# Kernel tuning notes

Measured on AMD Instinct MI355X. Metric: run time of the kernel, lower is better.

Reference implementation:

```python
import jax, jax.numpy as jnp
import numpy as np

ENC = 768
DEC = 768
B, T, S = 16, 1024, 1024


def setup_inputs() -> dict:
    key = jax.random.key(0)
    k1, k2, k3 = jax.random.split(key, 3)
    inputs = jax.random.normal(k1, (B, T, DEC), dtype=jnp.float32)
    context = jax.random.normal(k2, (B, S, ENC), dtype=jnp.float32)
    # linear_out: Linear(dec+enc -> dec) with bias; torch weight layout [out, in]
    W_out = jax.random.normal(k3, (DEC, DEC + ENC), dtype=jnp.float32) * 0.02
    b_out = jnp.zeros((DEC,), dtype=jnp.float32)
    w_scale = jnp.ones((1, 1, 1), dtype=jnp.float32)   # self.weight
    b_scale = jnp.ones((1, 1, 1), dtype=jnp.float32)   # self.bias
    prelu_a = jnp.full((1,), 0.25, dtype=jnp.float32)  # PReLU single param
    return {"inputs": inputs, "context": context, "W_out": W_out,
            "b_out": b_out, "w_scale": w_scale, "b_scale": b_scale,
            "prelu_a": prelu_a}


def reference(inputs, context, W_out, b_out, w_scale, b_scale, prelu_a):
    # score: bmm(h_t, h_s^T). NOTE: linear_in output is discarded in the
    # original (h_t reassigned), so the raw inputs are used — faithful here.
    align = jnp.einsum('btd,bsd->bts', inputs, context)        # [B,T,S]
    av = jax.nn.softmax(align, axis=-1)                        # softmax over src
    # gate: sigmoid of per-source column-sum over target positions
    gate = jax.nn.sigmoid(jnp.sum(av, axis=1, keepdims=True))  # [B,1,S]
    # AdaptiveAvgPool1d(1): mean over last (src) dim -> [B,T,1]
    pooled = jnp.mean(av, axis=-1, keepdims=True)
    av_g = av * gate * pooled                                  # fused elementwise
    c = jnp.einsum('bts,bsd->btd', av_g, context)              # [B,T,ENC]
    c = c * w_scale + b_scale                                  # scalar affine
    concat_c = jnp.concatenate([c, inputs], axis=-1)           # [B,T,ENC+DEC]
    h = jnp.einsum('btk,dk->btd', concat_c, W_out) + b_out     # linear_out
    attn_h = jnp.where(h >= 0, h, prelu_a * h)                 # PReLU
    return attn_h.transpose(1, 0, 2), av_g.transpose(1, 0, 2)
```

## Files before the change

kernel.cpp:

```cpp
#include <hip/hip_runtime.h>

#define B_ 16
#define T_ 1024
#define S_ 1024
#define D_ 768
#define K3_ 1536
#define BS_ (B_ * S_)
#define BD_ (B_ * D_)
#define NI_ (B_ * T_ * D_)
#define NW_ (D_ * K3_)

typedef __attribute__((ext_vector_type(8))) _Float16 half8;
typedef __attribute__((ext_vector_type(4))) float float4v;

__device__ __forceinline__ unsigned short f2h(float x) {
    return __builtin_bit_cast(unsigned short, (_Float16)x);
}
__device__ __forceinline__ float h2f(unsigned short u) {
    return (float)__builtin_bit_cast(_Float16, u);
}
__device__ __forceinline__ unsigned pkh2(float a, float b) {
    return (unsigned)f2h(a) | ((unsigned)f2h(b) << 16);
}
__device__ __forceinline__ uint2 pkh4(const float4 v) {
    return make_uint2(pkh2(v.x, v.y), pkh2(v.z, v.w));
}

__device__ __forceinline__ void gl_lds16(const void* g, void* l) {
    __builtin_amdgcn_global_load_lds(
        (const __attribute__((address_space(1))) unsigned int*)g,
        (__attribute__((address_space(3))) unsigned int*)l,
        16, 0, 0);
}

#define MFMA_PROLOG() \
    const int tid  = threadIdx.x; \
    const int w    = tid >> 6; \
    const int wm   = (w >> 1) * 64; \
    const int wn   = (w & 1) * 64; \
    const int lane = tid & 63; \
    const int q    = lane >> 4; \
    const int lr   = lane & 15; \
    float4v acc[4][4] = {};

#define STAGE_PROLOG() \
    const int rl0 = (w << 5) + (lane >> 2); \
    const int cc  = (lane & 3) * 8; \
    unsigned short* const Aw0 = &As[w * 1024]; \
    unsigned short* const Aw1 = &As[w * 1024 + 512]; \
    unsigned short* const Bw0 = &Bs[w * 1024]; \
    unsigned short* const Bw1 = &Bs[w * 1024 + 512];

#define MFMA_COMPUTE_F16() \
    { \
        half8 afr[4], bfr[4]; \
        _Pragma("unroll") \
        for (int i = 0; i < 4; i++) \
            afr[i] = *(const half8*)&As[(wm + i * 16 + lr) * 32 + q * 8]; \
        _Pragma("unroll") \
        for (int j = 0; j < 4; j++) \
            bfr[j] = *(const half8*)&Bs[(wn + j * 16 + lr) * 32 + q * 8]; \
        _Pragma("unroll") \
        for (int i = 0; i < 4; i++) \
            _Pragma("unroll") \
            for (int j = 0; j < 4; j++) \
                acc[i][j] = __builtin_amdgcn_mfma_f32_16x16x32_f16( \
                    afr[i], bfr[j], acc[i][j], 0, 0, 0); \
    }

__global__ __launch_bounds__(256) void prep_all(
    const float* __restrict__ ctx, const float* __restrict__ inp,
    const float* __restrict__ W,
    unsigned short* __restrict__ ctxT, unsigned short* __restrict__ ctx_h,
    unsigned short* __restrict__ inp_h, unsigned short* __restrict__ W_h)
{
    __shared__ unsigned short Ts[64 * 68];
    const int bid = blockIdx.x;
    const int tid = threadIdx.x;
    if (bid < 3072) {
        const int b   = bid / 192;
        const int rem = bid - b * 192;
        const int d0  = (rem >> 4) * 64;
        const int s0  = (rem & 15) * 64;
        const int srel = tid >> 4;
        const int dcol = (tid & 15) * 4;
#pragma unroll
        for (int r = 0; r < 4; r++) {
            const int s = srel + r * 16;
            float4 v = *(const float4*)(ctx + ((size_t)b * S_ + s0 + s) * D_ + d0 + dcol);
            Ts[(dcol + 0) * 68 + s] = f2h(v.x);
            Ts[(dcol + 1) * 68 + s] = f2h(v.y);
            Ts[(dcol + 2) * 68 + s] = f2h(v.z);
            Ts[(dcol + 3) * 68 + s] = f2h(v.w);
            *(uint2*)(ctx_h + ((size_t)b * S_ + s0 + s) * D_ + d0 + dcol) = pkh4(v);
        }
        __syncthreads();
        const int drow = tid >> 2;
        const int scg  = (tid & 3) * 16;
        unsigned short* dst = ctxT + ((size_t)b * D_ + d0 + drow) * S_ + s0 + scg;
#pragma unroll
        for (int p = 0; p < 4; p++) {
            uint2 u = *(const uint2*)&Ts[drow * 68 + scg + p * 4];
            *(uint2*)(dst + p * 4) = u;
        }
    } else {
        const size_t i4 = (size_t)(bid - 3072) * 256 + tid;
        const size_t flat = i4 * 4;
        float4 v;
        unsigned short* dst;
        if (flat < NI_) {
            v = ((const float4*)inp)[i4];
            dst = inp_h + flat;
        } else {
            v = *(const float4*)(W + (flat - NI_));
            dst = W_h + (flat - NI_);
        }
        *(uint2*)dst = pkh4(v);
    }
}

__global__ __launch_bounds__(256) void gemm_scores_f16(
    const unsigned short* __restrict__ ctx_h,
    const unsigned short* __restrict__ inp_h,
    float* __restrict__ out2)
{
    const int b  = blockIdx.z;
    const int t0 = blockIdx.y * 128;
    const int s0 = blockIdx.x * 128;

    __shared__ __align__(16) unsigned short As[128 * 32];
    __shared__ __align__(16) unsigned short Bs[128 * 32];

    MFMA_PROLOG();
    STAGE_PROLOG();

    const unsigned short* ga0 = ctx_h + ((size_t)b * S_ + s0 + rl0) * D_ + cc;
    const unsigned short* ga1 = ga0 + (size_t)16 * D_;
    const unsigned short* gb0 = inp_h + ((size_t)b * T_ + t0 + rl0) * D_ + cc;
    const unsigned short* gb1 = gb0 + (size_t)16 * D_;

    for (int kb = 0; kb < D_; kb += 32) {
        __syncthreads();
        gl_lds16(ga0 + kb, Aw0);
        gl_lds16(ga1 + kb, Aw1);
        gl_lds16(gb0 + kb, Bw0);
        gl_lds16(gb1 + kb, Bw1);
        __syncthreads();
        MFMA_COMPUTE_F16();
    }

#pragma unroll
    for (int i = 0; i < 4; i++)
#pragma unroll
        for (int j = 0; j < 4; j++) {
            const int t = t0 + wn + j * 16 + lr;
            const int s = s0 + wm + i * 16 + q * 4;
            *(float4v*)(out2 + (size_t)t * BS_ + (size_t)b * S_ + s) = acc[i][j];
        }
}

__global__ __launch_bounds__(256) void softmax_rows(
    const float* __restrict__ scores, unsigned short* __restrict__ av_h)
{
    const int bid = blockIdx.x;
    const int b = bid & (B_ - 1);
    const int t = bid / B_;
    const float* row = scores + (size_t)t * BS_ + (size_t)b * S_;
    const int tid = threadIdx.x;

    float4 v = ((const float4*)row)[tid];
    float m = fmaxf(fmaxf(v.x, v.y), fmaxf(v.z, v.w));
#pragma unroll
    for (int off = 32; off > 0; off >>= 1) m = fmaxf(m, __shfl_xor(m, off));

    __shared__ float red[8];
    if ((tid & 63) == 0) red[tid >> 6] = m;
    __syncthreads();
    m = fmaxf(fmaxf(red[0], red[1]), fmaxf(red[2], red[3]));

    float4 e;
    e.x = __expf(v.x - m); e.y = __expf(v.y - m);
    e.z = __expf(v.z - m); e.w = __expf(v.w - m);
    float s = e.x + e.y + e.z + e.w;
#pragma unroll
    for (int off = 32; off > 0; off >>= 1) s += __shfl_xor(s, off);
    if ((tid & 63) == 0) red[4 + (tid >> 6)] = s;
    __syncthreads();
    s = (red[4] + red[5]) + (red[6] + red[7]);

    const float inv = 1.0f / s;
    e.x *= inv; e.y *= inv; e.z *= inv; e.w *= inv;
    unsigned short* orow = av_h + (size_t)t * BS_ + (size_t)b * S_;
    *(uint2*)(orow + tid * 4) = pkh4(e);
}

__global__ __launch_bounds__(256) void colsum_part(
    const unsigned short* __restrict__ av_h, float* __restrict__ partial)
{
    const int b = blockIdx.y;
    const int c = blockIdx.z;
    const int s2 = blockIdx.x * 512 + threadIdx.x * 2;
    const unsigned short* p = av_h + (size_t)(c * 128) * BS_ + (size_t)b * S_ + s2;
    float s0 = 0.0f, s1 = 0.0f;
#pragma unroll 8
    for (int t = 0; t < 128; t++) {
        const unsigned u = *(const unsigned*)(p + (size_t)t * BS_);
        s0 += h2f((unsigned short)(u & 0xffff));
        s1 += h2f((unsigned short)(u >> 16));
    }
    *(float2*)(partial + ((size_t)c * B_ + b) * S_ + s2) = make_float2(s0, s1);
}

__global__ __launch_bounds__(256) void gate_final(
    const float* __restrict__ partial, float* __restrict__ gate)
{
    const int idx = blockIdx.x * 256 + threadIdx.x;
    const int b = idx >> 10, s = idx & (S_ - 1);
    float sum = 0.0f;
#pragma unroll
    for (int c = 0; c < T_ / 128; c++) sum += partial[((size_t)c * B_ + b) * S_ + s];
    gate[idx] = (1.0f / (1.0f + __expf(-sum))) * (1.0f / (float)S_);
}

__global__ __launch_bounds__(256) void av_out(
    const unsigned short* __restrict__ av_h, const float* __restrict__ gate,
    float* __restrict__ out2)
{
    const size_t i8 = ((size_t)blockIdx.x * 256 + threadIdx.x) * 8;
    const int s = (int)(i8 & (S_ - 1));
    const int b = (int)((i8 >> 10) & (B_ - 1));
    const uint4 u = *(const uint4*)(av_h + i8);
    const float4 g0 = *(const float4*)(gate + b * S_ + s);
    const float4 g1 = *(const float4*)(gate + b * S_ + s + 4);
    float4 o0 = make_float4(h2f(u.x & 0xffff) * g0.x, h2f(u.x >> 16) * g0.y,
                            h2f(u.y & 0xffff) * g0.z, h2f(u.y >> 16) * g0.w);
    float4 o1 = make_float4(h2f(u.z & 0xffff) * g1.x, h2f(u.z >> 16) * g1.y,
                            h2f(u.w & 0xffff) * g1.z, h2f(u.w >> 16) * g1.w);
    *(float4*)(out2 + i8) = o0;
    *(float4*)(out2 + i8 + 4) = o1;
}

__global__ __launch_bounds__(256) void scale_ctxT(
    unsigned short* __restrict__ ctxT, const float* __restrict__ gate)
{
    const int b = blockIdx.y;
    const int d = blockIdx.x * 2 + (threadIdx.x >> 7);
    const int s = (threadIdx.x & 127) * 8;
    unsigned short* p = ctxT + ((size_t)b * D_ + d) * S_ + s;
    const uint4 u = *(const uint4*)p;
    const float4 g0 = *(const float4*)(gate + b * S_ + s);
    const float4 g1 = *(const float4*)(gate + b * S_ + s + 4);
    uint4 o;
    o.x = pkh2(h2f(u.x & 0xffff) * g0.x, h2f(u.x >> 16) * g0.y);
    o.y = pkh2(h2f(u.y & 0xffff) * g0.z, h2f(u.y >> 16) * g0.w);
    o.z = pkh2(h2f(u.z & 0xffff) * g1.x, h2f(u.z >> 16) * g1.y);
    o.w = pkh2(h2f(u.w & 0xffff) * g1.z, h2f(u.w >> 16) * g1.w);
    *(uint4*)p = o;
}

__global__ __launch_bounds__(256) void gemm_ctx_f16(
    const unsigned short* __restrict__ ctxT, const unsigned short* __restrict__ av_h,
    const float* __restrict__ w_scale, const float* __restrict__ b_scale,
    unsigned short* __restrict__ c_h)
{
    const int b  = blockIdx.z;
    const int d0 = blockIdx.y * 128;
    const int t0 = blockIdx.x * 128;

    __shared__ __align__(16) unsigned short As[128 * 32];
    __shared__ __align__(16) unsigned short Bs[128 * 32];

    MFMA_PROLOG();
    STAGE_PROLOG();

    const unsigned short* ga0 = ctxT + ((size_t)b * D_ + d0 + rl0) * S_ + cc;
    const unsigned short* ga1 = ga0 + (size_t)16 * S_;
    const unsigned short* gb0 = av_h + (size_t)(t0 + rl0) * BS_ + (size_t)b * S_ + cc;
    const unsigned short* gb1 = gb0 + (size_t)16 * BS_;

    for (int sb = 0; sb < S_; sb += 32) {
        __syncthreads();
        gl_lds16(ga0 + sb, Aw0);
        gl_lds16(ga1 + sb, Aw1);
        gl_lds16(gb0 + sb, Bw0);
        gl_lds16(gb1 + sb, Bw1);
        __syncthreads();
        MFMA_COMPUTE_F16();
    }

    const float wsc = w_scale[0], bsc = b_scale[0];
#pragma unroll
    for (int i = 0; i < 4; i++)
#pragma unroll
        for (int j = 0; j < 4; j++) {
            const int d = d0 + wm + i * 16 + q * 4;
            const int t = t0 + wn + j * 16 + lr;
            uint2 o;
            o.x = pkh2(acc[i][j][0] * wsc + bsc, acc[i][j][1] * wsc + bsc);
            o.y = pkh2(acc[i][j][2] * wsc + bsc, acc[i][j][3] * wsc + bsc);
            *(uint2*)(c_h + ((size_t)b * T_ + t) * D_ + d) = o;
        }
}

__global__ __launch_bounds__(256) void gemm_out_f16(
    const unsigned short* __restrict__ c_h, const unsigned short* __restrict__ inp_h,
    const unsigned short* __restrict__ W_h, const float* __restrict__ bias,
    const float* __restrict__ prelu_a, float* __restrict__ out0)
{
    const int n0 = blockIdx.x * 128;
    const int d0 = blockIdx.y * 128;

    __shared__ __align__(16) unsigned short As[128 * 32];
    __shared__ __align__(16) unsigned short Bs[128 * 32];

    MFMA_PROLOG();
    STAGE_PROLOG();

    const unsigned short* ga0  = W_h + (size_t)(d0 + rl0) * K3_ + cc;
    const unsigned short* ga1  = ga0 + (size_t)16 * K3_;
    const unsigned short* gbc0 = c_h + (size_t)(n0 + rl0) * D_ + cc;
    const unsigned short* gbi0 = inp_h + (size_t)(n0 + rl0) * D_ + cc;

    for (int kb = 0; kb < K3_; kb += 32) {
        const unsigned short* gb0 = (kb < D_) ? gbc0 + kb : gbi0 + (kb - D_);
        const unsigned short* gb1 = gb0 + (size_t)16 * D_;
        __syncthreads();
        gl_lds16(ga0 + kb, Aw0);
        gl_lds16(ga1 + kb, Aw1);
        gl_lds16(gb0, Bw0);
        gl_lds16(gb1, Bw1);
        __syncthreads();
        MFMA_COMPUTE_F16();
    }

    const float pa = prelu_a[0];
#pragma unroll
    for (int i = 0; i < 4; i++) {
        const int d = d0 + wm + i * 16 + q * 4;
        const float4 bz = *(const float4*)(bias + d);
#pragma unroll
        for (int j = 0; j < 4; j++) {
            const int n = n0 + wn + j * 16 + lr;
            const int bb = n >> 10;
            const int t = n & (T_ - 1);
            float4 h;
            h.x = acc[i][j][0] + bz.x;
            h.y = acc[i][j][1] + bz.y;
            h.z = acc[i][j][2] + bz.z;
            h.w = acc[i][j][3] + bz.w;
            h.x = h.x >= 0.0f ? h.x : pa * h.x;
            h.y = h.y >= 0.0f ? h.y : pa * h.y;
            h.z = h.z >= 0.0f ? h.z : pa * h.z;
            h.w = h.w >= 0.0f ? h.w : pa * h.w;
            *(float4*)(out0 + (size_t)t * BD_ + (size_t)bb * D_ + d) = h;
        }
    }
}

extern "C" void kernel_launch(void* const* d_in, const int* in_sizes, int n_in,
                              void* d_out, int out_size, void* d_ws, size_t ws_size,
                              hipStream_t stream)
{
    const float* inputs  = (const float*)d_in[0];
    const float* context = (const float*)d_in[1];
    const float* W_out   = (const float*)d_in[2];
    const float* b_out   = (const float*)d_in[3];
    const float* w_scale = (const float*)d_in[4];
    const float* b_scale = (const float*)d_in[5];
    const float* prelu_a = (const float*)d_in[6];

    float* out0 = (float*)d_out;
    float* out2 = out0 + (size_t)T_ * B_ * D_;

    unsigned short* c_h   = (unsigned short*)d_ws;
    unsigned short* ctxT  = c_h   + (size_t)B_ * T_ * D_;
    unsigned short* av_h  = ctxT  + (size_t)B_ * D_ * S_;
    unsigned short* inp_h = av_h  + (size_t)T_ * B_ * S_;
    unsigned short* W_h   = inp_h + (size_t)B_ * T_ * D_;
    float* gate    = (float*)(W_h + (size_t)NW_);
    float* partial = gate + (size_t)B_ * S_;

    prep_all<<<3072 + (NI_ + NW_) / 4 / 256, 256, 0, stream>>>(
        context, inputs, W_out, ctxT, c_h, inp_h, W_h);
    gemm_scores_f16<<<dim3(S_ / 128, T_ / 128, B_), 256, 0, stream>>>(
        c_h , inp_h, out2);
    softmax_rows<<<B_ * T_, 256, 0, stream>>>(out2, av_h);
    colsum_part<<<dim3(S_ / 512, B_, T_ / 128), 256, 0, stream>>>(av_h, partial);
    gate_final<<<(B_ * S_) / 256, 256, 0, stream>>>(partial, gate);
    av_out<<<(int)(((size_t)T_ * B_ * S_ / 8) / 256), 256, 0, stream>>>(av_h, gate, out2);
    scale_ctxT<<<dim3(D_ / 2, B_), 256, 0, stream>>>(ctxT, gate);
    gemm_ctx_f16<<<dim3(T_ / 128, D_ / 128, B_), 256, 0, stream>>>(
        ctxT, av_h, w_scale, b_scale, c_h);
    gemm_out_f16<<<dim3((B_ * T_) / 128, D_ / 128), 256, 0, stream>>>(
        c_h, inp_h, W_h, b_out, prelu_a, out0);
}
```

Before: 391.3 us.

## Double-buffer GEMM LDS staging, remap blocks across XCDs, fold gate into av

All three MFMA GEMMs now double-buffer their LDS tiles: the next k-slice is prefetched while the current one is computed, with a single barrier per iteration instead of two. Block indices are remapped so blocks sharing the same batch or row tiles are grouped onto the same XCD, which should improve L2 reuse. The scale_ctxT kernel is removed: av_out writes the gated fp16 av back into av_h, so the context GEMM consumes the gate through av rather than through a rescaled ctxT, and the 1/S factor moves into the epilogue. This costs an extra fp16 write in av_out and doubles shared memory per block, which may reduce occupancy.

```diff
diff --git a/kernel.cpp b/kernel.cpp
--- a/kernel.cpp
+++ b/kernel.cpp
@@ -46,20 +46,17 @@
 #define STAGE_PROLOG() \
     const int rl0 = (w << 5) + (lane >> 2); \
     const int cc  = (lane & 3) * 8; \
-    unsigned short* const Aw0 = &As[w * 1024]; \
-    unsigned short* const Aw1 = &As[w * 1024 + 512]; \
-    unsigned short* const Bw0 = &Bs[w * 1024]; \
-    unsigned short* const Bw1 = &Bs[w * 1024 + 512];
-
-#define MFMA_COMPUTE_F16() \
+    const int wb  = w * 1024;
+
+#define MFMA_COMPUTE_F16(AS, BS) \
     { \
         half8 afr[4], bfr[4]; \
         _Pragma("unroll") \
         for (int i = 0; i < 4; i++) \
-            afr[i] = *(const half8*)&As[(wm + i * 16 + lr) * 32 + q * 8]; \
+            afr[i] = *(const half8*)&(AS)[(wm + i * 16 + lr) * 32 + q * 8]; \
         _Pragma("unroll") \
         for (int j = 0; j < 4; j++) \
-            bfr[j] = *(const half8*)&Bs[(wn + j * 16 + lr) * 32 + q * 8]; \
+            bfr[j] = *(const half8*)&(BS)[(wn + j * 16 + lr) * 32 + q * 8]; \
         _Pragma("unroll") \
         for (int i = 0; i < 4; i++) \
             _Pragma("unroll") \
@@ -124,12 +121,14 @@
     const unsigned short* __restrict__ inp_h,
     float* __restrict__ out2)
 {
-    const int b  = blockIdx.z;
-    const int t0 = blockIdx.y * 128;
-    const int s0 = blockIdx.x * 128;
-
-    __shared__ __align__(16) unsigned short As[128 * 32];
-    __shared__ __align__(16) unsigned short Bs[128 * 32];
+    const int hwid = blockIdx.x + (blockIdx.y << 3) + (blockIdx.z << 6);
+    const int wk   = (hwid & 7) * 128 + (hwid >> 3);
+    const int b  = wk >> 6;
+    const int t0 = ((wk >> 3) & 7) * 128;
+    const int s0 = (wk & 7) * 128;
+
+    __shared__ __align__(16) unsigned short As[2][128 * 32];
+    __shared__ __align__(16) unsigned short Bs[2][128 * 32];
 
     MFMA_PROLOG();
     STAGE_PROLOG();
@@ -139,15 +138,24 @@
     const unsigned short* gb0 = inp_h + ((size_t)b * T_ + t0 + rl0) * D_ + cc;
     const unsigned short* gb1 = gb0 + (size_t)16 * D_;
 
-    for (int kb = 0; kb < D_; kb += 32) {
+    gl_lds16(ga0, &As[0][wb]);
+    gl_lds16(ga1, &As[0][wb + 512]);
+    gl_lds16(gb0, &Bs[0][wb]);
+    gl_lds16(gb1, &Bs[0][wb + 512]);
+    __syncthreads();
+
+    int cur = 0;
+    for (int kb = 32; kb < D_; kb += 32) {
+        const int nxt = cur ^ 1;
+        gl_lds16(ga0 + kb, &As[nxt][wb]);
+        gl_lds16(ga1 + kb, &As[nxt][wb + 512]);
+        gl_lds16(gb0 + kb, &Bs[nxt][wb]);
+        gl_lds16(gb1 + kb, &Bs[nxt][wb + 512]);
+        MFMA_COMPUTE_F16(As[cur], Bs[cur]);
         __syncthreads();
-        gl_lds16(ga0 + kb, Aw0);
-        gl_lds16(ga1 + kb, Aw1);
-        gl_lds16(gb0 + kb, Bw0);
-        gl_lds16(gb1 + kb, Bw1);
-        __syncthreads();
-        MFMA_COMPUTE_F16();
-    }
+        cur = nxt;
+    }
+    MFMA_COMPUTE_F16(As[cur], Bs[cur]);
 
 #pragma unroll
     for (int i = 0; i < 4; i++)
@@ -219,11 +227,11 @@
     float sum = 0.0f;
 #pragma unroll
     for (int c = 0; c < T_ / 128; c++) sum += partial[((size_t)c * B_ + b) * S_ + s];
-    gate[idx] = (1.0f / (1.0f + __expf(-sum))) * (1.0f / (float)S_);
+    gate[idx] = 1.0f / (1.0f + __expf(-sum));
 }
 
 __global__ __launch_bounds__(256) void av_out(
-    const unsigned short* __restrict__ av_h, const float* __restrict__ gate,
+    unsigned short* __restrict__ av_h, const float* __restrict__ gate,
     float* __restrict__ out2)
 {
     const size_t i8 = ((size_t)blockIdx.x * 256 + threadIdx.x) * 8;
@@ -232,30 +240,17 @@
     const uint4 u = *(const uint4*)(av_h + i8);
     const float4 g0 = *(const float4*)(gate + b * S_ + s);
     const float4 g1 = *(const float4*)(gate + b * S_ + s + 4);
-    float4 o0 = make_float4(h2f(u.x & 0xffff) * g0.x, h2f(u.x >> 16) * g0.y,
-                            h2f(u.y & 0xffff) * g0.z, h2f(u.y >> 16) * g0.w);
-    float4 o1 = make_float4(h2f(u.z & 0xffff) * g1.x, h2f(u.z >> 16) * g1.y,
-                            h2f(u.w & 0xffff) * g1.z, h2f(u.w >> 16) * g1.w);
-    *(float4*)(out2 + i8) = o0;
-    *(float4*)(out2 + i8 + 4) = o1;
-}
-
-__global__ __launch_bounds__(256) void scale_ctxT(
-    unsigned short* __restrict__ ctxT, const float* __restrict__ gate)
-{
-    const int b = blockIdx.y;
-    const int d = blockIdx.x * 2 + (threadIdx.x >> 7);
-    const int s = (threadIdx.x & 127) * 8;
-    unsigned short* p = ctxT + ((size_t)b * D_ + d) * S_ + s;
-    const uint4 u = *(const uint4*)p;
-    const float4 g0 = *(const float4*)(gate + b * S_ + s);
-    const float4 g1 = *(const float4*)(gate + b * S_ + s + 4);
+    float a0 = h2f(u.x & 0xffff) * g0.x, a1 = h2f(u.x >> 16) * g0.y;
+    float a2 = h2f(u.y & 0xffff) * g0.z, a3 = h2f(u.y >> 16) * g0.w;
+    float a4 = h2f(u.z & 0xffff) * g1.x, a5 = h2f(u.z >> 16) * g1.y;
+    float a6 = h2f(u.w & 0xffff) * g1.z, a7 = h2f(u.w >> 16) * g1.w;
+    const float is = 1.0f / (float)S_;
+    *(float4*)(out2 + i8)     = make_float4(a0 * is, a1 * is, a2 * is, a3 * is);
+    *(float4*)(out2 + i8 + 4) = make_float4(a4 * is, a5 * is, a6 * is, a7 * is);
     uint4 o;
-    o.x = pkh2(h2f(u.x & 0xffff) * g0.x, h2f(u.x >> 16) * g0.y);
-    o.y = pkh2(h2f(u.y & 0xffff) * g0.z, h2f(u.y >> 16) * g0.w);
-    o.z = pkh2(h2f(u.z & 0xffff) * g1.x, h2f(u.z >> 16) * g1.y);
-    o.w = pkh2(h2f(u.w & 0xffff) * g1.z, h2f(u.w >> 16) * g1.w);
-    *(uint4*)p = o;
+    o.x = pkh2(a0, a1); o.y = pkh2(a2, a3);
+    o.z = pkh2(a4, a5); o.w = pkh2(a6, a7);
+    *(uint4*)(av_h + i8) = o;
 }
 
 __global__ __launch_bounds__(256) void gemm_ctx_f16(
@@ -263,12 +258,14 @@
     const float* __restrict__ w_scale, const float* __restrict__ b_scale,
     unsigned short* __restrict__ c_h)
 {
-    const int b  = blockIdx.z;
-    const int d0 = blockIdx.y * 128;
-    const int t0 = blockIdx.x * 128;
-
-    __shared__ __align__(16) unsigned short As[128 * 32];
-    __shared__ __align__(16) unsigned short Bs[128 * 32];
+    const int hwid = blockIdx.x + blockIdx.y * 8 + blockIdx.z * 48;
+    const int wk   = (hwid & 7) * 96 + (hwid >> 3);
+    const int t0 = (wk % 8) * 128;
+    const int d0 = ((wk / 8) % 6) * 128;
+    const int b  = wk / 48;
+
+    __shared__ __align__(16) unsigned short As[2][128 * 32];
+    __shared__ __align__(16) unsigned short Bs[2][128 * 32];
 
     MFMA_PROLOG();
     STAGE_PROLOG();
@@ -278,17 +275,27 @@
     const unsigned short* gb0 = av_h + (size_t)(t0 + rl0) * BS_ + (size_t)b * S_ + cc;
     const unsigned short* gb1 = gb0 + (size_t)16 * BS_;
 
-    for (int sb = 0; sb < S_; sb += 32) {
+    gl_lds16(ga0, &As[0][wb]);
+    gl_lds16(ga1, &As[0][wb + 512]);
+    gl_lds16(gb0, &Bs[0][wb]);
+    gl_lds16(gb1, &Bs[0][wb + 512]);
+    __syncthreads();
+
+    int cur = 0;
+    for (int sb = 32; sb < S_; sb += 32) {
+        const int nxt = cur ^ 1;
+        gl_lds16(ga0 + sb, &As[nxt][wb]);
+        gl_lds16(ga1 + sb, &As[nxt][wb + 512]);
+        gl_lds16(gb0 + sb, &Bs[nxt][wb]);
+        gl_lds16(gb1 + sb, &Bs[nxt][wb + 512]);
+        MFMA_COMPUTE_F16(As[cur], Bs[cur]);
         __syncthreads();
-        gl_lds16(ga0 + sb, Aw0);
-        gl_lds16(ga1 + sb, Aw1);
-        gl_lds16(gb0 + sb, Bw0);
-        gl_lds16(gb1 + sb, Bw1);
-        __syncthreads();
-        MFMA_COMPUTE_F16();
-    }
-
-    const float wsc = w_scale[0], bsc = b_scale[0];
+        cur = nxt;
+    }
+    MFMA_COMPUTE_F16(As[cur], Bs[cur]);
+
+    const float wsc = w_scale[0] * (1.0f / (float)S_);
+    const float bsc = b_scale[0];
 #pragma unroll
     for (int i = 0; i < 4; i++)
 #pragma unroll
@@ -307,11 +314,13 @@
     const unsigned short* __restrict__ W_h, const float* __restrict__ bias,
     const float* __restrict__ prelu_a, float* __restrict__ out0)
 {
-    const int n0 = blockIdx.x * 128;
-    const int d0 = blockIdx.y * 128;
-
-    __shared__ __align__(16) unsigned short As[128 * 32];
-    __shared__ __align__(16) unsigned short Bs[128 * 32];
+    const int hwid = blockIdx.x + blockIdx.y * 6;
+    const int wk   = (hwid & 7) * 96 + (hwid >> 3);
+    const int d0 = (wk % 6) * 128;
+    const int n0 = (wk / 6) * 128;
+
+    __shared__ __align__(16) unsigned short As[2][128 * 32];
+    __shared__ __align__(16) unsigned short Bs[2][128 * 32];
 
     MFMA_PROLOG();
     STAGE_PROLOG();
@@ -321,17 +330,25 @@
     const unsigned short* gbc0 = c_h + (size_t)(n0 + rl0) * D_ + cc;
     const unsigned short* gbi0 = inp_h + (size_t)(n0 + rl0) * D_ + cc;
 
-    for (int kb = 0; kb < K3_; kb += 32) {
+    gl_lds16(ga0, &As[0][wb]);
+    gl_lds16(ga1, &As[0][wb + 512]);
+    gl_lds16(gbc0, &Bs[0][wb]);
+    gl_lds16(gbc0 + (size_t)16 * D_, &Bs[0][wb + 512]);
+    __syncthreads();
+
+    int cur = 0;
+    for (int kb = 32; kb < K3_; kb += 32) {
+        const int nxt = cur ^ 1;
         const unsigned short* gb0 = (kb < D_) ? gbc0 + kb : gbi0 + (kb - D_);
-        const unsigned short* gb1 = gb0 + (size_t)16 * D_;
+        gl_lds16(ga0 + kb, &As[nxt][wb]);
+        gl_lds16(ga1 + kb, &As[nxt][wb + 512]);
+        gl_lds16(gb0, &Bs[nxt][wb]);
+        gl_lds16(gb0 + (size_t)16 * D_, &Bs[nxt][wb + 512]);
+        MFMA_COMPUTE_F16(As[cur], Bs[cur]);
         __syncthreads();
-        gl_lds16(ga0 + kb, Aw0);
-        gl_lds16(ga1 + kb, Aw1);
-        gl_lds16(gb0, Bw0);
-        gl_lds16(gb1, Bw1);
-        __syncthreads();
-        MFMA_COMPUTE_F16();
-    }
+        cur = nxt;
+    }
+    MFMA_COMPUTE_F16(As[cur], Bs[cur]);
 
     const float pa = prelu_a[0];
 #pragma unroll
@@ -387,10 +404,10 @@
     softmax_rows<<<B_ * T_, 256, 0, stream>>>(out2, av_h);
     colsum_part<<<dim3(S_ / 512, B_, T_ / 128), 256, 0, stream>>>(av_h, partial);
     gate_final<<<(B_ * S_) / 256, 256, 0, stream>>>(partial, gate);
-    av_out<<<(int)(((size_t)T_ * B_ * S_ / 8) / 256), 256, 0, stream>>>(av_h, gate, out2);
-    scale_ctxT<<<dim3(D_ / 2, B_), 256, 0, stream>>>(ctxT, gate);
+    av_out<<<(int)(((size_t)T_ * B_ * S_ / 8) / 256), 256, 0, stream>>>(
+        av_h, gate, out2);
     gemm_ctx_f16<<<dim3(T_ / 128, D_ / 128, B_), 256, 0, stream>>>(
         ctxT, av_h, w_scale, b_scale, c_h);
-    gemm_out_f16<<<dim3((B_ * T_) / 128, D_ / 128), 256, 0, stream>>>(
+    gemm_out_f16<<<dim3(D_ / 128, (B_ * T_) / 128), 256, 0, stream>>>(
         c_h, inp_h, W_h, b_out, prelu_a, out0);
 }
```

Measured after the change: 384.1 us. No clear change (-1.8%).
